# Kernel tuning notes

Hardware: AMD Instinct MI355X
Metric: run time of the kernel (lower is better)

## Reference

```python
import jax, jax.numpy as jnp
import numpy as np

HEADS = 8
DIM_HEAD = 32


def setup_inputs() -> dict:
    key = jax.random.key(0)
    k1, k2, k3 = jax.random.split(key, 3)
    dim = 256
    hd = HEADS * DIM_HEAD  # 256
    x = jax.random.normal(k1, (2, dim, 16, 64, 64), dtype=jnp.float32)
    w_qkv = jax.random.normal(k2, (3 * hd, dim), dtype=jnp.float32) * (1.0 / np.sqrt(dim))
    w_out = jax.random.normal(k3, (dim, hd), dtype=jnp.float32) * (1.0 / np.sqrt(hd))
    b_out = jnp.zeros((dim,), dtype=jnp.float32)
    return {"x": x, "w_qkv": w_qkv, "w_out": w_out, "b_out": b_out}


def reference(x, w_qkv, w_out, b_out):
    b, c, f, h, w = x.shape
    n = h * w
    scale = DIM_HEAD ** (-0.5)
    # (b c f h w) -> ((b f) c (h w))
    xr = jnp.transpose(x, (0, 2, 1, 3, 4)).reshape(b * f, c, n)
    # 1x1 conv (no bias) == channel GEMM
    qkv = jnp.einsum('oc,bcn->bon', w_qkv, xr)  # (bf, 3*H*D, n)
    q, k, v = jnp.split(qkv, 3, axis=1)
    def heads(t):
        return t.reshape(b * f, HEADS, DIM_HEAD, n)
    q, k, v = heads(q), heads(k), heads(v)
    q = jax.nn.softmax(q, axis=-2) * scale   # softmax over feature dim d
    k = jax.nn.softmax(k, axis=-1)           # softmax over spatial dim n
    context = jnp.einsum('bhdn,bhen->bhde', k, v)   # (bf, H, D, D)
    out = jnp.einsum('bhde,bhdn->bhen', context, q)  # (bf, H, D, n)
    out = out.reshape(b * f, HEADS * DIM_HEAD, n)
    out = jnp.einsum('oc,bcn->bon', w_out, out) + b_out[None, :, None]
    # ((b f) c (h w)) -> (b c f h w)
    out = out.reshape(b, f, c, h, w)
    return jnp.transpose(out, (0, 2, 1, 3, 4))
```

## Files before the change

### kernel.cpp

```cpp
#include <hip/hip_runtime.h>
#include <cmath>


typedef unsigned short u16;
typedef __attribute__((ext_vector_type(4))) unsigned short u16x4;
typedef __attribute__((ext_vector_type(8))) unsigned short u16x8;
typedef __attribute__((ext_vector_type(4))) unsigned int   u32x4;
typedef __attribute__((ext_vector_type(8))) short bf16x8;
typedef __attribute__((ext_vector_type(4))) float f32x4;

#define XCH_STRIDE 65536
#define XB_STRIDE  16777216

__device__ __forceinline__ float bf2f(u16 u) {
    union { unsigned int i; float f; } w; w.i = ((unsigned int)u) << 16; return w.f;
}
__device__ __forceinline__ u16 f2bf(float f) {
    union { float f; unsigned int i; } w; w.f = f;
    return (u16)((w.i + 0x7FFFu + ((w.i >> 16) & 1u)) >> 16);
}
__device__ __forceinline__ void async16(const void* g, void* l) {
    __builtin_amdgcn_global_load_lds(
        (const __attribute__((address_space(1))) unsigned int*)g,
        (__attribute__((address_space(3))) unsigned int*)l, 16, 0, 0);
}

__global__ __launch_bounds__(256) void k_cvt_x(const float* __restrict__ x,
                                               u16* __restrict__ xbf, int fr0)
{
    const int tid = threadIdx.x;
    const int n0 = blockIdx.x * 64;
    const int c0 = blockIdx.y * 64;
    const int fl = blockIdx.z;
    const int frame = fr0 + fl, b = frame >> 4, f = frame & 15;
    const float* xb = x + (size_t)b * XB_STRIDE + (size_t)f * 4096;
    __shared__ float T[64][65];
    const int nn = tid & 63, cq = tid >> 6;
    #pragma unroll
    for (int r = 0; r < 16; ++r) {
        const int cl = r * 4 + cq;
        T[cl][nn] = xb[(size_t)(c0 + cl) * XCH_STRIDE + n0 + nn];
    }
    __syncthreads();
    const int jl = tid >> 2, c16 = (tid & 3) * 16;
    u16* dst = xbf + ((size_t)fl * 4096 + n0 + jl) * 256 + c0 + c16;
    u16x8 a, bv;
    #pragma unroll
    for (int i = 0; i < 8; ++i) a[i] = f2bf(T[c16 + i][jl]);
    #pragma unroll
    for (int i = 0; i < 8; ++i) bv[i] = f2bf(T[c16 + 8 + i][jl]);
    *(u16x8*)dst = a;
    *(u16x8*)(dst + 8) = bv;
}

__global__ __launch_bounds__(256) void k_cvt_w(const float* __restrict__ w,
                                               u16* __restrict__ wbf)
{
    const int i = (blockIdx.x * 256 + threadIdx.x) * 8;
    u16x8 o;
    #pragma unroll
    for (int j = 0; j < 8; ++j) o[j] = f2bf(w[i + j]);
    *(u16x8*)(wbf + i) = o;
}

__global__ __launch_bounds__(256) void k_qkv_mfma(const u16* __restrict__ xbf,
                                                  const u16* __restrict__ wq,
                                                  u16* __restrict__ qkv)
{
    const int tid = threadIdx.x;
    const int lane = tid & 63, wave = tid >> 6;
    const int ln = lane & 15, quad = lane >> 4;
    const int wm = wave & 1, wn = wave >> 1;

    const int chunk = gridDim.x >> 3;
    const int newid = (blockIdx.x & 7) * chunk + (blockIdx.x >> 3);
    const int o0 = (newid % 6) * 128;
    const int j0 = (newid / 6) * 128;

    __shared__ __align__(16) u16 sm[128 * 136];

    f32x4 acc[4][4] = {};
    const int lrow = lane >> 2;
    const int lk8 = ((lane & 3) ^ ((lrow >> 1) & 3)) * 8;
    const int sw8 = (quad ^ ((ln >> 1) & 3)) * 8;

    const u16* gB = xbf + (size_t)j0 * 256;
    const int r0 = wave * 32 + lrow;
    const u16* gA0 = wq + (size_t)(o0 + wm * 64 + ln) * 256 + quad * 8;

    bf16x8 afr[2][4];

    async16(gB + (size_t)r0 * 256 + lk8,        sm + (wave*2) * 512);
    async16(gB + (size_t)(r0+16) * 256 + lk8,   sm + (wave*2+1) * 512);
    #pragma unroll
    for (int mi = 0; mi < 4; ++mi)
        afr[0][mi] = *(const bf16x8*)(gA0 + mi * 16 * 256);
    async16(gB + (size_t)r0 * 256 + 32 + lk8,      sm + 4096 + (wave*2) * 512);
    async16(gB + (size_t)(r0+16) * 256 + 32 + lk8, sm + 4096 + (wave*2+1) * 512);
    asm volatile("s_waitcnt vmcnt(2)\n\ts_barrier" ::: "memory");

    #pragma unroll
    for (int t = 0; t < 8; ++t) {
        const u16* Bs = sm + (t % 3) * 4096;
        if (t < 6) {
            u16* Bn = sm + ((t + 2) % 3) * 4096;
            const int kk2 = (t + 2) * 32;
            async16(gB + (size_t)r0 * 256 + kk2 + lk8,      Bn + (wave*2) * 512);
            async16(gB + (size_t)(r0+16) * 256 + kk2 + lk8, Bn + (wave*2+1) * 512);
        }
        if (t < 7) {
            const int kk1 = (t + 1) * 32;
            #pragma unroll
            for (int mi = 0; mi < 4; ++mi)
                afr[(t + 1) & 1][mi] = *(const bf16x8*)(gA0 + mi * 16 * 256 + kk1);
        }
        bf16x8 bfv[4];
        #pragma unroll
        for (int ni = 0; ni < 4; ++ni)
            bfv[ni] = *(const bf16x8*)&Bs[(wn * 64 + ni * 16 + ln) * 32 + sw8];
        #pragma unroll
        for (int mi = 0; mi < 4; ++mi)
            #pragma unroll
            for (int ni = 0; ni < 4; ++ni)
                acc[mi][ni] = __builtin_amdgcn_mfma_f32_16x16x32_bf16(
                    afr[t & 1][mi], bfv[ni], acc[mi][ni], 0, 0, 0);
        if (t < 6)       asm volatile("s_waitcnt vmcnt(6)\n\ts_barrier" ::: "memory");
        else if (t == 6) asm volatile("s_waitcnt vmcnt(4)\n\ts_barrier" ::: "memory");
    }

    __syncthreads();
    u16* outl = sm;
    #pragma unroll
    for (int mi = 0; mi < 4; ++mi)
        #pragma unroll
        for (int ni = 0; ni < 4; ++ni) {
            const int jl = wn * 64 + ni * 16 + ln;
            const int ob = wm * 64 + mi * 16 + quad * 4;
            u16x4 u;
            u[0] = f2bf(acc[mi][ni][0]); u[1] = f2bf(acc[mi][ni][1]);
            u[2] = f2bf(acc[mi][ni][2]); u[3] = f2bf(acc[mi][ni][3]);
            *(u16x4*)&outl[jl * 136 + ob] = u;
        }
    __syncthreads();

    if (o0 < 256) {
        #pragma unroll
        for (int t = 0; t < 2; ++t) {
            const int idx = t * 256 + tid;
            const int r = idx >> 2, hh = idx & 3;
            const u16* p = &outl[r * 136 + hh * 32];
            float v[32];
            float m = -1e30f;
            #pragma unroll
            for (int g = 0; g < 4; ++g) {
                u16x8 u = *(const u16x8*)(p + g * 8);
                #pragma unroll
                for (int i = 0; i < 8; ++i) {
                    v[g * 8 + i] = bf2f(u[i]);
                    m = fmaxf(m, v[g * 8 + i]);
                }
            }
            float s = 0.f;
            #pragma unroll
            for (int i = 0; i < 32; ++i) { v[i] = __expf(v[i] - m); s += v[i]; }
            const float inv = 0.17677669529663687f / s;
            u16* q = qkv + (size_t)(j0 + r) * 768 + o0 + hh * 32;
            #pragma unroll
            for (int g = 0; g < 4; ++g) {
                u16x8 ov;
                #pragma unroll
                for (int i = 0; i < 8; ++i) ov[i] = f2bf(v[g * 8 + i] * inv);
                *(u16x8*)(q + g * 8) = ov;
            }
        }
    } else {
        #pragma unroll
        for (int r = 0; r < 8; ++r) {
            const int row = r * 16 + (tid >> 4);
            const int cb = (tid & 15) * 8;
            u32x4 v = *(const u32x4*)&outl[row * 136 + cb];
            *(u32x4*)(qkv + (size_t)(j0 + row) * 768 + o0 + cb) = v;
        }
    }
}

__global__ __launch_bounds__(256) void k_kstat1(const u16* __restrict__ qkv,
                                                float* __restrict__ sp)
{
    const int js = blockIdx.x, fl = blockIdx.y;
    const int tid = threadIdx.x;
    const int s = tid >> 5, g = tid & 31;
    const u16* base = qkv + ((size_t)fl * 4096 + js * 256 + s) * 768 + 256 + g * 8;
    float m[8], sm[8];
    #pragma unroll
    for (int i = 0; i < 8; ++i) { m[i] = -1e30f; sm[i] = 0.f; }
    for (int it = 0; it < 32; ++it) {
        u16x8 u = *(const u16x8*)(base + (size_t)it * 8 * 768);
        #pragma unroll
        for (int i = 0; i < 8; ++i) {
            float v = bf2f(u[i]);
            float nm = fmaxf(m[i], v);
            sm[i] = sm[i] * __expf(m[i] - nm) + __expf(v - nm);
            m[i] = nm;
        }
    }
    __shared__ float Lm[8][256], Ls[8][256];
    #pragma unroll
    for (int i = 0; i < 8; ++i) { Lm[s][g * 8 + i] = m[i]; Ls[s][g * 8 + i] = sm[i]; }
    __syncthreads();
    const int col = tid;
    float M = -1e30f;
    #pragma unroll
    for (int k = 0; k < 8; ++k) M = fmaxf(M, Lm[k][col]);
    float S = 0.f;
    #pragma unroll
    for (int k = 0; k < 8; ++k) S += Ls[k][col] * __expf(Lm[k][col] - M);
    float* o = sp + (((size_t)fl * 16 + js) * 256 + col) * 2;
    o[0] = M; o[1] = S;
}

__global__ __launch_bounds__(256) void k_kstat2(const float* __restrict__ sp,
                                                float* __restrict__ stat)
{
    const int fl = blockIdx.x, col = threadIdx.x;
    float mv[16], sv[16];
    float M = -1e30f;
    #pragma unroll
    for (int js = 0; js < 16; ++js) {
        const float* p = sp + (((size_t)fl * 16 + js) * 256 + col) * 2;
        mv[js] = p[0]; sv[js] = p[1];
        M = fmaxf(M, mv[js]);
    }
    float S = 0.f;
    #pragma unroll
    for (int js = 0; js < 16; ++js) S += sv[js] * __expf(mv[js] - M);
    float* o = stat + ((size_t)fl * 256 + col) * 2;
    o[0] = M; o[1] = 1.0f / S;
}

__global__ __launch_bounds__(256) void k_ctx(const u16* __restrict__ qkv,
                                             const float* __restrict__ stat,
                                             float* __restrict__ P)
{
    const int js = blockIdx.x, fl = blockIdx.y;
    const int tid = threadIdx.x;
    const int ls = tid >> 5, lg = tid & 31;
    const int h = tid >> 5, dg = (tid >> 3) & 3, eg = tid & 7;
    const int d0 = dg * 8, e0 = eg * 4;

    float Mg[8];
    #pragma unroll
    for (int i = 0; i < 8; ++i) Mg[i] = stat[((size_t)fl * 256 + lg * 8 + i) * 2];

    __shared__ float expk[8][264], vbuf[8][264];
    f32x4 acc[8] = {};
    const u16* kbase = qkv + ((size_t)fl * 4096 + js * 256 + ls) * 768 + 256 + lg * 8;

    for (int ch = 0; ch < 32; ++ch) {
        const u16* kp = kbase + (size_t)ch * 8 * 768;
        u16x8 ku = *(const u16x8*)kp;
        u16x8 vu = *(const u16x8*)(kp + 256);
        __syncthreads();
        #pragma unroll
        for (int i = 0; i < 8; ++i) {
            expk[ls][lg * 8 + i] = __expf(bf2f(ku[i]) - Mg[i]);
            vbuf[ls][lg * 8 + i] = bf2f(vu[i]);
        }
        __syncthreads();
        #pragma unroll
        for (int rr = 0; rr < 8; ++rr) {
            f32x4 w0 = *(const f32x4*)&expk[rr][h * 32 + d0];
            f32x4 w1 = *(const f32x4*)&expk[rr][h * 32 + d0 + 4];
            f32x4 vv = *(const f32x4*)&vbuf[rr][h * 32 + e0];
            #pragma unroll
            for (int ei = 0; ei < 4; ++ei) {
                acc[0][ei] = fmaf(w0[0], vv[ei], acc[0][ei]);
                acc[1][ei] = fmaf(w0[1], vv[ei], acc[1][ei]);
                acc[2][ei] = fmaf(w0[2], vv[ei], acc[2][ei]);
                acc[3][ei] = fmaf(w0[3], vv[ei], acc[3][ei]);
                acc[4][ei] = fmaf(w1[0], vv[ei], acc[4][ei]);
                acc[5][ei] = fmaf(w1[1], vv[ei], acc[5][ei]);
                acc[6][ei] = fmaf(w1[2], vv[ei], acc[6][ei]);
                acc[7][ei] = fmaf(w1[3], vv[ei], acc[7][ei]);
            }
        }
    }
    float* o = P + ((size_t)fl * 16 + js) * 8192 + (h * 32 + d0) * 32 + e0;
    #pragma unroll
    for (int di = 0; di < 8; ++di) *(f32x4*)(o + di * 32) = acc[di];
}

__global__ __launch_bounds__(256) void k_w2fold(const float* __restrict__ P,
                                                const float* __restrict__ stat,
                                                const float* __restrict__ w_out,
                                                u16* __restrict__ w2)
{
    const int h = blockIdx.x, fl = blockIdx.y;
    const int tid = threadIdx.x;
    __shared__ float Cs[32 * 33];

    const float* p0 = P + (size_t)fl * 16 * 8192 + h * 1024 + tid * 4;
    f32x4 sum = {0.f, 0.f, 0.f, 0.f};
    #pragma unroll
    for (int js = 0; js < 16; ++js) {
        f32x4 v = *(const f32x4*)(p0 + (size_t)js * 8192);
        sum[0] += v[0]; sum[1] += v[1]; sum[2] += v[2]; sum[3] += v[3];
    }
    const int d = tid >> 3, e4 = (tid & 7) * 4;
    const float inv = stat[((size_t)fl * 256 + h * 32 + d) * 2 + 1];
    Cs[d * 33 + e4 + 0] = sum[0] * inv;
    Cs[d * 33 + e4 + 1] = sum[1] * inv;
    Cs[d * 33 + e4 + 2] = sum[2] * inv;
    Cs[d * 33 + e4 + 3] = sum[3] * inv;
    __syncthreads();

    const int o = tid;
    float a2[32];
    #pragma unroll
    for (int dd = 0; dd < 32; ++dd) a2[dd] = 0.f;
    for (int e = 0; e < 32; ++e) {
        const float wv = w_out[(size_t)o * 256 + h * 32 + e];
        #pragma unroll
        for (int dd = 0; dd < 32; ++dd) a2[dd] = fmaf(wv, Cs[dd * 33 + e], a2[dd]);
    }
    u16* wp = w2 + (size_t)fl * 65536 + (size_t)o * 256 + h * 32;
    #pragma unroll
    for (int g = 0; g < 4; ++g) {
        u16x8 ov;
        #pragma unroll
        for (int i = 0; i < 8; ++i) ov[i] = f2bf(a2[g * 8 + i]);
        *(u16x8*)(wp + g * 8) = ov;
    }
}

__global__ __launch_bounds__(256) void k_out_mfma(const u16* __restrict__ qkv,
                                                  const u16* __restrict__ w2,
                                                  const float* __restrict__ b_out,
                                                  float* __restrict__ out, int fr0)
{
    const int tid = threadIdx.x;
    const int lane = tid & 63, wave = tid >> 6;
    const int ln = lane & 15, quad = lane >> 4;
    const int wm = wave & 1, wn = wave >> 1;

    const int chunk = gridDim.x >> 3;
    const int newid = (blockIdx.x & 7) * chunk + (blockIdx.x >> 3);
    const int o0 = (newid & 1) * 128;
    const int j0 = (newid >> 1) * 128;

    const int fl = j0 >> 12;
    const int frame = fr0 + fl, b = frame >> 4, f = frame & 15;
    const int nb = j0 & 4095;
    const u16* w2f = w2 + (size_t)fl * 65536;

    __shared__ __align__(16) u16 sm[12288];

    f32x4 acc[4][4] = {};
    const int lrow = lane >> 2;
    const int lk8 = ((lane & 3) ^ ((lrow >> 1) & 3)) * 8;
    const int sw8 = (quad ^ ((ln >> 1) & 3)) * 8;

    const u16* gA = qkv + (size_t)j0 * 768;
    const int r0 = wave * 32 + lrow;
    const u16* gB0 = w2f + (size_t)(o0 + wn * 64 + ln) * 256 + quad * 8;

    bf16x8 bfr[2][4];

    async16(gA + (size_t)r0 * 768 + lk8,        sm + (wave*2) * 512);
    async16(gA + (size_t)(r0+16) * 768 + lk8,   sm + (wave*2+1) * 512);
    #pragma unroll
    for (int ni = 0; ni < 4; ++ni)
        bfr[0][ni] = *(const bf16x8*)(gB0 + ni * 16 * 256);
    async16(gA + (size_t)r0 * 768 + 32 + lk8,      sm + 4096 + (wave*2) * 512);
    async16(gA + (size_t)(r0+16) * 768 + 32 + lk8, sm + 4096 + (wave*2+1) * 512);
    asm volatile("s_waitcnt vmcnt(2)\n\ts_barrier" ::: "memory");

    #pragma unroll
    for (int t = 0; t < 8; ++t) {
        const u16* As = sm + (t % 3) * 4096;
        if (t < 6) {
            u16* An = sm + ((t + 2) % 3) * 4096;
            const int kk2 = (t + 2) * 32;
            async16(gA + (size_t)r0 * 768 + kk2 + lk8,      An + (wave*2) * 512);
            async16(gA + (size_t)(r0+16) * 768 + kk2 + lk8, An + (wave*2+1) * 512);
        }
        if (t < 7) {
            const int kk1 = (t + 1) * 32;
            #pragma unroll
            for (int ni = 0; ni < 4; ++ni)
                bfr[(t + 1) & 1][ni] = *(const bf16x8*)(gB0 + ni * 16 * 256 + kk1);
        }
        bf16x8 af[4];
        #pragma unroll
        for (int mi = 0; mi < 4; ++mi)
            af[mi] = *(const bf16x8*)&As[(wm * 64 + mi * 16 + ln) * 32 + sw8];
        #pragma unroll
        for (int mi = 0; mi < 4; ++mi)
            #pragma unroll
            for (int ni = 0; ni < 4; ++ni)
                acc[mi][ni] = __builtin_amdgcn_mfma_f32_16x16x32_bf16(
                    af[mi], bfr[t & 1][ni], acc[mi][ni], 0, 0, 0);
        if (t < 6)       asm volatile("s_waitcnt vmcnt(6)\n\ts_barrier" ::: "memory");
        else if (t == 6) asm volatile("s_waitcnt vmcnt(4)\n\ts_barrier" ::: "memory");
    }

    float* obase = out + (size_t)b * XB_STRIDE + (size_t)f * 4096;
    #pragma unroll
    for (int ni = 0; ni < 4; ++ni) {
        const int o = o0 + wn * 64 + ni * 16 + ln;
        const float bias = b_out[o];
        #pragma unroll
        for (int mi = 0; mi < 4; ++mi) {
            const int jn = nb + wm * 64 + mi * 16 + quad * 4;
            f32x4 v = acc[mi][ni];
            v[0] += bias; v[1] += bias; v[2] += bias; v[3] += bias;
            *(f32x4*)(obase + (size_t)o * XCH_STRIDE + jn) = v;
        }
    }
}

extern "C" void kernel_launch(void* const* d_in, const int* in_sizes, int n_in,
                              void* d_out, int out_size, void* d_ws, size_t ws_size,
                              hipStream_t stream)
{
    const float* x     = (const float*)d_in[0];
    const float* w_qkv = (const float*)d_in[1];
    const float* w_out = (const float*)d_in[2];
    const float* b_out = (const float*)d_in[3];
    float* out = (float*)d_out;

    const size_t per_frame = (size_t)4096 * 256 * 2 + (size_t)4096 * 768 * 2
                           + 65536 * 2 + 16 * 512 * 4 + 512 * 4 + 16 * 8192 * 4;
    const size_t wq_bytes = 768 * 256 * 2;
    int CF = 32;
    while (CF > 1 && (size_t)CF * per_frame + wq_bytes > ws_size) CF >>= 1;

    u16* wq_bf  = (u16*)d_ws;
    u16* xbf    = wq_bf + 768 * 256;
    u16* qkv    = xbf + (size_t)CF * 4096 * 256;
    u16* w2     = qkv + (size_t)CF * 4096 * 768;
    float* sp   = (float*)(w2 + (size_t)CF * 65536);
    float* stat = sp + (size_t)CF * 16 * 256 * 2;
    float* P    = stat + (size_t)CF * 256 * 2;

    k_cvt_w<<<96, 256, 0, stream>>>(w_qkv, wq_bf);
    for (int fr0 = 0; fr0 < 32; fr0 += CF) {
        k_cvt_x   <<<dim3(64, 4, CF), 256, 0, stream>>>(x, xbf, fr0);
        k_qkv_mfma<<<CF * 32 * 6, 256, 0, stream>>>(xbf, wq_bf, qkv);
        k_kstat1  <<<dim3(16, CF), 256, 0, stream>>>(qkv, sp);
        k_kstat2  <<<CF, 256, 0, stream>>>(sp, stat);
        k_ctx     <<<dim3(16, CF), 256, 0, stream>>>(qkv, stat, P);
        k_w2fold  <<<dim3(8, CF), 256, 0, stream>>>(P, stat, w_out, w2);
        k_out_mfma<<<CF * 32 * 2, 256, 0, stream>>>(qkv, w2, b_out, out, fr0);
    }
}
```

Before: 518.2 us.

## Pre-swizzle weight matrices into MFMA fragment order for coalesced register loads

The bf16 weight conversion and the per-frame w2 producer now write weights in a fragment-major layout, so each wave's direct-to-register operand loads read 64 contiguous 16-byte chunks instead of strided rows. Both GEMM kernels index this layout and issue the register prefetch before the LDS async copies. The aim is fewer memory transactions for the weight operand. The cost is more complex indexing in the producer kernels, whose global writes or reads become scattered.

```diff
diff --git a/kernel.cpp b/kernel.cpp
--- a/kernel.cpp
+++ b/kernel.cpp
@@ -54,13 +54,21 @@
 }
 
 __global__ __launch_bounds__(256) void k_cvt_w(const float* __restrict__ w,
-                                               u16* __restrict__ wbf)
-{
-    const int i = (blockIdx.x * 256 + threadIdx.x) * 8;
+                                               u16* __restrict__ wf)
+{
+    const int idx = blockIdx.x * 256 + threadIdx.x;
+    const int l   = idx & 63;
+    const int mi  = (idx >> 6) & 3;
+    const int wm  = (idx >> 8) & 1;
+    const int kk  = (idx >> 9) & 7;
+    const int ob  = idx >> 12;
+    const int row = ob * 128 + wm * 64 + mi * 16 + (l & 15);
+    const int col = kk * 32 + (l >> 4) * 8;
+    const float* src = w + (size_t)row * 256 + col;
     u16x8 o;
     #pragma unroll
-    for (int j = 0; j < 8; ++j) o[j] = f2bf(w[i + j]);
-    *(u16x8*)(wbf + i) = o;
+    for (int j = 0; j < 8; ++j) o[j] = f2bf(src[j]);
+    *(u16x8*)(wf + (size_t)idx * 8) = o;
 }
 
 __global__ __launch_bounds__(256) void k_qkv_mfma(const u16* __restrict__ xbf,
@@ -86,7 +94,7 @@
 
     const u16* gB = xbf + (size_t)j0 * 256;
     const int r0 = wave * 32 + lrow;
-    const u16* gA0 = wq + (size_t)(o0 + wm * 64 + ln) * 256 + quad * 8;
+    const u16* gAf = wq + (size_t)(o0 >> 7) * 32768 + wm * 2048 + lane * 8;
 
     bf16x8 afr[2][4];
 
@@ -94,26 +102,26 @@
     async16(gB + (size_t)(r0+16) * 256 + lk8,   sm + (wave*2+1) * 512);
     #pragma unroll
     for (int mi = 0; mi < 4; ++mi)
-        afr[0][mi] = *(const bf16x8*)(gA0 + mi * 16 * 256);
+        afr[0][mi] = *(const bf16x8*)(gAf + mi * 512);
     async16(gB + (size_t)r0 * 256 + 32 + lk8,      sm + 4096 + (wave*2) * 512);
     async16(gB + (size_t)(r0+16) * 256 + 32 + lk8, sm + 4096 + (wave*2+1) * 512);
     asm volatile("s_waitcnt vmcnt(2)\n\ts_barrier" ::: "memory");
 
     #pragma unroll
     for (int t = 0; t < 8; ++t) {
-        const u16* Bs = sm + (t % 3) * 4096;
+        if (t < 7) {
+            #pragma unroll
+            for (int mi = 0; mi < 4; ++mi)
+                afr[(t+1) & 1][mi] =
+                    *(const bf16x8*)(gAf + (t+1) * 4096 + mi * 512);
+        }
         if (t < 6) {
             u16* Bn = sm + ((t + 2) % 3) * 4096;
             const int kk2 = (t + 2) * 32;
             async16(gB + (size_t)r0 * 256 + kk2 + lk8,      Bn + (wave*2) * 512);
             async16(gB + (size_t)(r0+16) * 256 + kk2 + lk8, Bn + (wave*2+1) * 512);
         }
-        if (t < 7) {
-            const int kk1 = (t + 1) * 32;
-            #pragma unroll
-            for (int mi = 0; mi < 4; ++mi)
-                afr[(t + 1) & 1][mi] = *(const bf16x8*)(gA0 + mi * 16 * 256 + kk1);
-        }
+        const u16* Bs = sm + (t % 3) * 4096;
         bf16x8 bfv[4];
         #pragma unroll
         for (int ni = 0; ni < 4; ++ni)
@@ -323,13 +331,16 @@
         #pragma unroll
         for (int dd = 0; dd < 32; ++dd) a2[dd] = fmaf(wv, Cs[dd * 33 + e], a2[dd]);
     }
-    u16* wp = w2 + (size_t)fl * 65536 + (size_t)o * 256 + h * 32;
+    const int ob = o >> 7, rr = o & 127;
+    const int wn = rr >> 6, ni = (rr >> 4) & 3, lnn = rr & 15;
+    u16* wp = w2 + (size_t)fl * 65536
+                 + (size_t)((((ob * 8 + h) * 2 + wn) * 4 + ni) * 64) * 8;
     #pragma unroll
     for (int g = 0; g < 4; ++g) {
         u16x8 ov;
         #pragma unroll
         for (int i = 0; i < 8; ++i) ov[i] = f2bf(a2[g * 8 + i]);
-        *(u16x8*)(wp + g * 8) = ov;
+        *(u16x8*)(wp + (size_t)(g * 16 + lnn) * 8) = ov;
     }
 }
 
@@ -362,7 +373,7 @@
 
     const u16* gA = qkv + (size_t)j0 * 768;
     const int r0 = wave * 32 + lrow;
-    const u16* gB0 = w2f + (size_t)(o0 + wn * 64 + ln) * 256 + quad * 8;
+    const u16* gBf = w2f + (size_t)(o0 >> 7) * 32768 + wn * 2048 + lane * 8;
 
     bf16x8 bfr[2][4];
 
@@ -370,26 +381,26 @@
     async16(gA + (size_t)(r0+16) * 768 + lk8,   sm + (wave*2+1) * 512);
     #pragma unroll
     for (int ni = 0; ni < 4; ++ni)
-        bfr[0][ni] = *(const bf16x8*)(gB0 + ni * 16 * 256);
+        bfr[0][ni] = *(const bf16x8*)(gBf + ni * 512);
     async16(gA + (size_t)r0 * 768 + 32 + lk8,      sm + 4096 + (wave*2) * 512);
     async16(gA + (size_t)(r0+16) * 768 + 32 + lk8, sm + 4096 + (wave*2+1) * 512);
     asm volatile("s_waitcnt vmcnt(2)\n\ts_barrier" ::: "memory");
 
     #pragma unroll
     for (int t = 0; t < 8; ++t) {
-        const u16* As = sm + (t % 3) * 4096;
+        if (t < 7) {
+            #pragma unroll
+            for (int ni = 0; ni < 4; ++ni)
+                bfr[(t+1) & 1][ni] =
+                    *(const bf16x8*)(gBf + (t+1) * 4096 + ni * 512);
+        }
         if (t < 6) {
             u16* An = sm + ((t + 2) % 3) * 4096;
             const int kk2 = (t + 2) * 32;
             async16(gA + (size_t)r0 * 768 + kk2 + lk8,      An + (wave*2) * 512);
             async16(gA + (size_t)(r0+16) * 768 + kk2 + lk8, An + (wave*2+1) * 512);
         }
-        if (t < 7) {
-            const int kk1 = (t + 1) * 32;
-            #pragma unroll
-            for (int ni = 0; ni < 4; ++ni)
-                bfr[(t + 1) & 1][ni] = *(const bf16x8*)(gB0 + ni * 16 * 256 + kk1);
-        }
+        const u16* As = sm + (t % 3) * 4096;
         bf16x8 af[4];
         #pragma unroll
         for (int mi = 0; mi < 4; ++mi)
```

Measured after the change: 470.4 us. 9.2% less time.
